# Optimization experiments

Hardware: AMD Instinct MI355X
Metric: run time of the kernel (lower is better)

The kernel has to match this reference:

```python
import jax, jax.numpy as jnp
import numpy as np

RADIUS = 0.2
K = 32  # num_neighbors


def setup_inputs() -> dict:
    key = jax.random.key(0)
    k1, k2, k3 = jax.random.split(key, 3)
    points_xyz = jax.random.uniform(k1, (2, 16384, 3), dtype=jnp.float32)
    center_xyz = jax.random.uniform(k2, (2, 2048, 3), dtype=jnp.float32)
    features = jax.random.normal(k3, (2, 64, 16384), dtype=jnp.float32)
    return {"points_xyz": points_xyz, "center_xyz": center_xyz, "features": features}


def _ball_query(center_xyz, points_xyz, k, radius):
    # squared distances (B, G, N) via ||c||^2 + ||p||^2 - 2 c.p (avoids (B,G,N,3) temp)
    c2 = jnp.sum(center_xyz * center_xyz, axis=-1)  # (B, G)
    p2 = jnp.sum(points_xyz * points_xyz, axis=-1)  # (B, N)
    cp = jnp.einsum('bgd,bnd->bgn', center_xyz, points_xyz)
    d2 = c2[:, :, None] + p2[:, None, :] - 2.0 * cp  # (B, G, N)
    n = points_xyz.shape[1]
    # key = point index if inside ball else sentinel N; first-K-in-ball == K smallest keys
    keys = jnp.where(d2 < radius * radius, jnp.arange(n, dtype=jnp.int32), n)
    neg_vals, _ = jax.lax.top_k(-keys, k)
    idx = -neg_vals  # (B, G, K) ascending point indices, sentinel n if <k found
    first = idx[..., :1]
    # pad missing slots with first found index (CUDA ball_query semantics), 0 if none
    idx = jnp.where(idx < n, idx, jnp.where(first < n, first, 0))
    return idx


def reference(points_xyz, center_xyz, features):
    idx = _ball_query(center_xyz, points_xyz, K, RADIUS)  # (B, G, K) int32
    gather = jax.vmap(lambda f, i: f[:, i])  # (C, N), (G, K) -> (C, G, K)
    grouped_xyz = gather(jnp.swapaxes(points_xyz, 1, 2), idx)  # (B, 3, G, K)
    # relative_xyz then normalize_xyz
    grouped_xyz = (grouped_xyz - jnp.swapaxes(center_xyz, 1, 2)[..., None]) / RADIUS
    grouped_features = gather(features, idx)  # (B, C, G, K)
    return grouped_xyz, grouped_features
```

## Files before the change

kernel.cpp:

```cpp
#include <hip/hip_runtime.h>
#include <hip/hip_bf16.h>

constexpr int NPTS = 16384;
constexpr int NCTR = 2048;
constexpr int NCH  = 64;
constexpr int KK   = 32;
constexpr int NB   = 2;
#define R2 0.04f

__global__ __launch_bounds__(256) void prep_kernel(
    const float* __restrict__ points,
    const float* __restrict__ centers,
    const float* __restrict__ feats,
    float* __restrict__ featsT,
    float* __restrict__ out_xyz,
    int* __restrict__ idx_out)
{
#pragma clang fp contract(off)
    __shared__ float tile[64][65];
    __shared__ int   s_idx[4][KK];

    if (blockIdx.x < 512) {
        const int b  = blockIdx.x >> 8;
        const int n0 = (blockIdx.x & 255) * 64;
        const int t  = threadIdx.x;
        const int nl = t & 63;
        const int q  = t >> 6;

        const float* fb = feats + (size_t)b * NCH * NPTS;
#pragma unroll
        for (int r = 0; r < 16; ++r) {
            int c = r * 4 + q;
            tile[c][nl] = fb[(size_t)c * NPTS + n0 + nl];
        }
        __syncthreads();
        float* ftb = featsT + ((size_t)b * NPTS + n0) * NCH;
#pragma unroll
        for (int r = 0; r < 16; ++r) {
            int n = r * 4 + q;
            ftb[(size_t)n * NCH + nl] = tile[nl][n];
        }
        return;
    }

    const int wave = threadIdx.x >> 6;
    const int lane = threadIdx.x & 63;
    const int cg   = (blockIdx.x - 512) * 4 + wave;
    const int b    = cg >> 11;
    const int g    = cg & (NCTR - 1);

    const float* pb = points + (size_t)b * NPTS * 3;
    const float* cc = centers + (size_t)cg * 3;
    const float cx = cc[0], cy = cc[1], cz = cc[2];
    const float c2 = (cx * cx + cy * cy) + cz * cz;

    int* idxs = s_idx[wave];

    float x[8], y[8], z[8], nx[8], ny[8], nz[8];
#pragma unroll
    for (int j = 0; j < 8; ++j) {
        const int i = j * 64 + lane;
        x[j] = pb[i * 3 + 0]; y[j] = pb[i * 3 + 1]; z[j] = pb[i * 3 + 2];
    }
    int cnt = 0;
    for (int base = 0; base < NPTS; base += 512) {
        const int nbb = (base + 512 < NPTS) ? base + 512 : 0;
#pragma unroll
        for (int j = 0; j < 8; ++j) {
            const int i = nbb + j * 64 + lane;
            nx[j] = pb[i * 3 + 0]; ny[j] = pb[i * 3 + 1]; nz[j] = pb[i * 3 + 2];
        }
#pragma unroll
        for (int j = 0; j < 8; ++j) {
            const float p2 = (x[j] * x[j] + y[j] * y[j]) + z[j] * z[j];
            const float cp = (cx * x[j] + cy * y[j]) + cz * z[j];
            const float d2 = (c2 + p2) - 2.0f * cp;
            const bool hit = d2 < R2;
            const unsigned long long m = __ballot(hit);
            if (hit) {
                const int slot = cnt + __popcll(m & ((1ull << lane) - 1ull));
                if (slot < KK) idxs[slot] = base + j * 64 + lane;
            }
            cnt += (int)__popcll(m);
        }
        if (cnt >= KK) break;
#pragma unroll
        for (int j = 0; j < 8; ++j) { x[j] = nx[j]; y[j] = ny[j]; z[j] = nz[j]; }
    }
    __syncthreads();

    const int cpd = cnt < KK ? cnt : KK;
    const int first = (cnt > 0) ? idxs[0] : 0;
    if (lane < KK) {
        const int id = (lane < cpd) ? idxs[lane] : first;
        idx_out[cg * KK + lane] = id;
        const float px = pb[id * 3 + 0];
        const float py = pb[id * 3 + 1];
        const float pz = pb[id * 3 + 2];
        const size_t ob = (((size_t)b * 3 + 0) * NCTR + g) * KK + lane;
        out_xyz[ob + (size_t)0 * NCTR * KK] = (px - cx) / 0.2f;
        out_xyz[ob + (size_t)1 * NCTR * KK] = (py - cy) / 0.2f;
        out_xyz[ob + (size_t)2 * NCTR * KK] = (pz - cz) / 0.2f;
    }
}

__global__ __launch_bounds__(256) void group_feats(
    const float* __restrict__ featsT,
    const int* __restrict__ idx_in,
    float* __restrict__ out_feat)
{
    __shared__ float sf[KK][68];
    __shared__ int   ids[KK];

    const int t  = threadIdx.x;
    const int cg = blockIdx.x;
    const int b  = cg >> 11;
    const int g  = cg & (NCTR - 1);

    if (t < KK) ids[t] = idx_in[cg * KK + t];
    __syncthreads();

    const int wave = t >> 6, lane = t & 63;
    const int li = lane & 15, r = lane >> 4;
    const float* ftb = featsT + (size_t)b * NPTS * NCH;
#pragma unroll
    for (int i = 0; i < 2; ++i) {
        const int k = wave * 8 + i * 4 + r;
        const float4 v = *((const float4*)(ftb + (size_t)ids[k] * NCH) + li);
        *(float4*)&sf[k][4 * li] = v;
    }
    __syncthreads();

    const int kq = t & 7;
    const int cL = t >> 3;
    const size_t ob = ((size_t)b * NCH * NCTR + g) * KK;
#pragma unroll
    for (int p = 0; p < 2; ++p) {
        const int c = cL + 32 * p;
        float4 v;
        v.x = sf[4 * kq + 0][c];
        v.y = sf[4 * kq + 1][c];
        v.z = sf[4 * kq + 2][c];
        v.w = sf[4 * kq + 3][c];
        *(float4*)(out_feat + ob + (size_t)c * NCTR * KK + 4 * kq) = v;
    }
}

__global__ __launch_bounds__(256) void ballquery_group(
    const float* __restrict__ points, const float* __restrict__ centers,
    const float* __restrict__ feats, float* __restrict__ out_xyz,
    float* __restrict__ out_feat)
{
#pragma clang fp contract(off)
    __shared__ int   s_idx[4][KK];
    __shared__ float s_f[4][KK][65];
    const int wave = threadIdx.x >> 6, lane = threadIdx.x & 63;
    const int cg = blockIdx.x * 4 + wave;
    const int b = cg >> 11, g = cg & (NCTR - 1);
    const float* pb = points + (size_t)b * NPTS * 3;
    const float* cc = centers + (size_t)cg * 3;
    const float cx = cc[0], cy = cc[1], cz = cc[2];
    const float c2 = (cx * cx + cy * cy) + cz * cz;
    int* idxs = s_idx[wave];
    int cnt = 0;
    for (int base = 0; base < NPTS; base += 64) {
        const int i = base + lane;
        const float px = pb[i * 3 + 0], py = pb[i * 3 + 1], pz = pb[i * 3 + 2];
        const float p2 = (px * px + py * py) + pz * pz;
        const float cp = (cx * px + cy * py) + cz * pz;
        const float d2 = (c2 + p2) - 2.0f * cp;
        const bool hit = d2 < R2;
        const unsigned long long m = __ballot(hit);
        if (hit) {
            const int slot = cnt + __popcll(m & ((1ull << lane) - 1ull));
            if (slot < KK) idxs[slot] = i;
        }
        cnt += (int)__popcll(m);
        if (cnt >= KK) break;
    }
    __syncthreads();
    const int cpd = cnt < KK ? cnt : KK;
    const int first = (cnt > 0) ? idxs[0] : 0;
    if (lane < KK) idxs[lane] = (lane < cpd) ? idxs[lane] : first;
    __syncthreads();
    if (lane < KK) {
        const int id = idxs[lane];
        const float px = pb[id * 3 + 0], py = pb[id * 3 + 1], pz = pb[id * 3 + 2];
        const size_t ob = (((size_t)b * 3 + 0) * NCTR + g) * KK + lane;
        out_xyz[ob + (size_t)0 * NCTR * KK] = (px - cx) / 0.2f;
        out_xyz[ob + (size_t)1 * NCTR * KK] = (py - cy) / 0.2f;
        out_xyz[ob + (size_t)2 * NCTR * KK] = (pz - cz) / 0.2f;
    }
    float (*sf)[65] = s_f[wave];
    const float* fb = feats + (size_t)b * NCH * NPTS;
    for (int k = 0; k < KK; ++k) {
        const int id = idxs[k];
        sf[k][lane] = fb[(size_t)lane * NPTS + id];
    }
    __syncthreads();
    const int k = lane & 31, ch = lane >> 5;
    const size_t ob = ((size_t)b * NCH * NCTR + g) * KK;
#pragma unroll
    for (int cc2 = 0; cc2 < 32; ++cc2) {
        const int c = cc2 * 2 + ch;
        out_feat[ob + (size_t)c * NCTR * KK + k] = sf[k][c];
    }
}

extern "C" void kernel_launch(void* const* d_in, const int* in_sizes, int n_in,
                              void* d_out, int out_size, void* d_ws, size_t ws_size,
                              hipStream_t stream) {
    const float* points  = (const float*)d_in[0];
    const float* centers = (const float*)d_in[1];
    const float* feats   = (const float*)d_in[2];

    float* out      = (float*)d_out;
    float* out_xyz  = out;
    float* out_feat = out + (size_t)NB * 3 * NCTR * KK;

    const size_t ftBytes  = (size_t)NB * NPTS * NCH * sizeof(float);
    const size_t idxBytes = (size_t)NB * NCTR * KK * sizeof(int);

    if (ws_size >= ftBytes + idxBytes) {
        float* featsT = (float*)d_ws;
        int*   idxbuf = (int*)((char*)d_ws + ftBytes);
        prep_kernel<<<1536, 256, 0, stream>>>(points, centers, feats,
                                              featsT, out_xyz, idxbuf);
        group_feats<<<NB * NCTR, 256, 0, stream>>>(featsT, idxbuf, out_feat);
    } else {
        ballquery_group<<<(NB * NCTR) / 4, 256, 0, stream>>>(
            points, centers, feats, out_xyz, out_feat);
    }
}
```

Baseline: 91.28 us.

## Pack points as float4 with norm and fuse ball query with feature grouping

The prep kernel now transposes features and also writes points packed as float4 (x, y, z, |p|^2). A new fused query_group kernel runs the ball query on the packed points, keeps the neighbor indices in shared memory, and gathers the transposed features in the same kernel. This removes the index buffer round trip, the separate group kernel launch, and the recomputation of p2, and it uses one vector load per point instead of three scalar loads. The cost is a dependency on the full transpose finishing before any query can start, more shared memory per block, and fewer parallel blocks for the gather phase.

```diff
diff --git a/kernel.cpp b/kernel.cpp
--- a/kernel.cpp
+++ b/kernel.cpp
@@ -10,15 +10,12 @@
 
 __global__ __launch_bounds__(256) void prep_kernel(
     const float* __restrict__ points,
-    const float* __restrict__ centers,
     const float* __restrict__ feats,
     float* __restrict__ featsT,
-    float* __restrict__ out_xyz,
-    int* __restrict__ idx_out)
+    float4* __restrict__ packed)
 {
 #pragma clang fp contract(off)
     __shared__ float tile[64][65];
-    __shared__ int   s_idx[4][KK];
 
     if (blockIdx.x < 512) {
         const int b  = blockIdx.x >> 8;
@@ -43,38 +40,55 @@
         return;
     }
 
+    const int tid = (blockIdx.x - 512) * 256 + threadIdx.x;
+#pragma unroll
+    for (int s = 0; s < 4; ++s) {
+        const int i = tid + s * 8192;
+        const float x = points[3 * i + 0];
+        const float y = points[3 * i + 1];
+        const float z = points[3 * i + 2];
+        const float p2 = (x * x + y * y) + z * z;
+        packed[i] = make_float4(x, y, z, p2);
+    }
+}
+
+__global__ __launch_bounds__(256, 4) void query_group(
+    const float4* __restrict__ packed,
+    const float* __restrict__ centers,
+    const float* __restrict__ featsT,
+    float* __restrict__ out_xyz,
+    float* __restrict__ out_feat)
+{
+#pragma clang fp contract(off)
+    __shared__ int   s_idx[4][KK];
+    __shared__ float s_f[4][KK][68];
+
     const int wave = threadIdx.x >> 6;
     const int lane = threadIdx.x & 63;
-    const int cg   = (blockIdx.x - 512) * 4 + wave;
+    const int cg   = blockIdx.x * 4 + wave;
     const int b    = cg >> 11;
     const int g    = cg & (NCTR - 1);
 
-    const float* pb = points + (size_t)b * NPTS * 3;
+    const float4* pk = packed + (size_t)b * NPTS;
     const float* cc = centers + (size_t)cg * 3;
     const float cx = cc[0], cy = cc[1], cz = cc[2];
     const float c2 = (cx * cx + cy * cy) + cz * cz;
 
     int* idxs = s_idx[wave];
 
-    float x[8], y[8], z[8], nx[8], ny[8], nz[8];
-#pragma unroll
-    for (int j = 0; j < 8; ++j) {
-        const int i = j * 64 + lane;
-        x[j] = pb[i * 3 + 0]; y[j] = pb[i * 3 + 1]; z[j] = pb[i * 3 + 2];
-    }
+    float4 cur[8], nxt[8];
+#pragma unroll
+    for (int j = 0; j < 8; ++j) cur[j] = pk[j * 64 + lane];
     int cnt = 0;
     for (int base = 0; base < NPTS; base += 512) {
         const int nbb = (base + 512 < NPTS) ? base + 512 : 0;
 #pragma unroll
+        for (int j = 0; j < 8; ++j) nxt[j] = pk[nbb + j * 64 + lane];
+#pragma unroll
         for (int j = 0; j < 8; ++j) {
-            const int i = nbb + j * 64 + lane;
-            nx[j] = pb[i * 3 + 0]; ny[j] = pb[i * 3 + 1]; nz[j] = pb[i * 3 + 2];
-        }
-#pragma unroll
-        for (int j = 0; j < 8; ++j) {
-            const float p2 = (x[j] * x[j] + y[j] * y[j]) + z[j] * z[j];
-            const float cp = (cx * x[j] + cy * y[j]) + cz * z[j];
-            const float d2 = (c2 + p2) - 2.0f * cp;
+            const float4 v = cur[j];
+            const float cp = (cx * v.x + cy * v.y) + cz * v.z;
+            const float d2 = (c2 + v.w) - 2.0f * cp;
             const bool hit = d2 < R2;
             const unsigned long long m = __ballot(hit);
             if (hit) {
@@ -85,7 +99,7 @@
         }
         if (cnt >= KK) break;
 #pragma unroll
-        for (int j = 0; j < 8; ++j) { x[j] = nx[j]; y[j] = ny[j]; z[j] = nz[j]; }
+        for (int j = 0; j < 8; ++j) cur[j] = nxt[j];
     }
     __syncthreads();
 
@@ -93,50 +107,32 @@
     const int first = (cnt > 0) ? idxs[0] : 0;
     if (lane < KK) {
         const int id = (lane < cpd) ? idxs[lane] : first;
-        idx_out[cg * KK + lane] = id;
-        const float px = pb[id * 3 + 0];
-        const float py = pb[id * 3 + 1];
-        const float pz = pb[id * 3 + 2];
+        idxs[lane] = id;
+        const float4 v = pk[id];
         const size_t ob = (((size_t)b * 3 + 0) * NCTR + g) * KK + lane;
-        out_xyz[ob + (size_t)0 * NCTR * KK] = (px - cx) / 0.2f;
-        out_xyz[ob + (size_t)1 * NCTR * KK] = (py - cy) / 0.2f;
-        out_xyz[ob + (size_t)2 * NCTR * KK] = (pz - cz) / 0.2f;
-    }
-}
-
-__global__ __launch_bounds__(256) void group_feats(
-    const float* __restrict__ featsT,
-    const int* __restrict__ idx_in,
-    float* __restrict__ out_feat)
-{
-    __shared__ float sf[KK][68];
-    __shared__ int   ids[KK];
-
-    const int t  = threadIdx.x;
-    const int cg = blockIdx.x;
-    const int b  = cg >> 11;
-    const int g  = cg & (NCTR - 1);
-
-    if (t < KK) ids[t] = idx_in[cg * KK + t];
-    __syncthreads();
-
-    const int wave = t >> 6, lane = t & 63;
+        out_xyz[ob + (size_t)0 * NCTR * KK] = (v.x - cx) / 0.2f;
+        out_xyz[ob + (size_t)1 * NCTR * KK] = (v.y - cy) / 0.2f;
+        out_xyz[ob + (size_t)2 * NCTR * KK] = (v.z - cz) / 0.2f;
+    }
+    __syncthreads();
+
+    float (*sf)[68] = s_f[wave];
     const int li = lane & 15, r = lane >> 4;
     const float* ftb = featsT + (size_t)b * NPTS * NCH;
 #pragma unroll
-    for (int i = 0; i < 2; ++i) {
-        const int k = wave * 8 + i * 4 + r;
-        const float4 v = *((const float4*)(ftb + (size_t)ids[k] * NCH) + li);
+    for (int i = 0; i < 8; ++i) {
+        const int k = i * 4 + r;
+        const float4 v = *((const float4*)(ftb + (size_t)idxs[k] * NCH) + li);
         *(float4*)&sf[k][4 * li] = v;
     }
     __syncthreads();
 
-    const int kq = t & 7;
-    const int cL = t >> 3;
+    const int kq = lane & 7;
+    const int c0 = lane >> 3;
     const size_t ob = ((size_t)b * NCH * NCTR + g) * KK;
 #pragma unroll
-    for (int p = 0; p < 2; ++p) {
-        const int c = cL + 32 * p;
+    for (int p = 0; p < 8; ++p) {
+        const int c = c0 + 8 * p;
         float4 v;
         v.x = sf[4 * kq + 0][c];
         v.y = sf[4 * kq + 1][c];
@@ -218,15 +214,15 @@
     float* out_xyz  = out;
     float* out_feat = out + (size_t)NB * 3 * NCTR * KK;
 
-    const size_t ftBytes  = (size_t)NB * NPTS * NCH * sizeof(float);
-    const size_t idxBytes = (size_t)NB * NCTR * KK * sizeof(int);
-
-    if (ws_size >= ftBytes + idxBytes) {
-        float* featsT = (float*)d_ws;
-        int*   idxbuf = (int*)((char*)d_ws + ftBytes);
-        prep_kernel<<<1536, 256, 0, stream>>>(points, centers, feats,
-                                              featsT, out_xyz, idxbuf);
-        group_feats<<<NB * NCTR, 256, 0, stream>>>(featsT, idxbuf, out_feat);
+    const size_t ftBytes = (size_t)NB * NPTS * NCH * sizeof(float);
+    const size_t pkBytes = (size_t)NB * NPTS * 4 * sizeof(float);
+
+    if (ws_size >= ftBytes + pkBytes) {
+        float*  featsT = (float*)d_ws;
+        float4* packed = (float4*)((char*)d_ws + ftBytes);
+        prep_kernel<<<544, 256, 0, stream>>>(points, feats, featsT, packed);
+        query_group<<<(NB * NCTR) / 4, 256, 0, stream>>>(
+            packed, centers, featsT, out_xyz, out_feat);
     } else {
         ballquery_group<<<(NB * NCTR) / 4, 256, 0, stream>>>(
             points, centers, feats, out_xyz, out_feat);
```

Result: faster. 86.23 us (-5.5%).
